# Kernel optimization log

Hardware: AMD Instinct MI355X
Metric: run time of the kernel (lower is better)

The kernel has to match this reference:

```python
import jax, jax.numpy as jnp
import numpy as np

START_TAG = 7
STOP_TAG = 8
NEG = -10000.0  # matches torch.full((1,K), -10000.) in the original


def setup_inputs() -> dict:
    key = jax.random.key(0)
    k1, k2, k3, k4 = jax.random.split(key, 4)
    B, T, K = 1024, 2048, 9  # K = output_dim + 2 (START/STOP hardcoded as 7/8)
    feats = jax.random.normal(k1, (B, T, K), dtype=jnp.float32)
    tags = jax.random.randint(k2, (B, T), 0, 7)            # valid labels 0..6
    lengths = jax.random.randint(k3, (B,), 1, T + 1)        # per-sentence lengths >= 1
    transitions = jax.random.normal(k4, (K, K), dtype=jnp.float32)
    transitions = transitions.at[START_TAG, :].set(NEG)     # never transition into START
    transitions = transitions.at[:, STOP_TAG].set(NEG)      # never transition out of STOP
    return {"feats": feats, "transitions": transitions, "tags": tags, "lengths": lengths}


def _crf_nll(feats, transitions, tags, lengths):
    # feats: [B,T,K] emissions, transitions[j,i] = score of i -> j
    B, T, K = feats.shape

    def fwd_one(feat, length):
        # CRF forward algorithm (log partition), vectorized over tags,
        # lax.scan over time; masked past `length` to emulate feats[:x_len].
        alpha0 = jnp.full((K,), NEG, feat.dtype).at[START_TAG].set(0.0)

        def step(alpha, inp):
            t, f = inp
            # alpha_new[j] = logsumexp_i(alpha[i] + transitions[j,i]) + feat[t,j]
            new = jax.nn.logsumexp(alpha[None, :] + transitions, axis=1) + f
            return jnp.where(t < length, new, alpha), None

        alpha, _ = jax.lax.scan(step, alpha0, (jnp.arange(T), feat))
        return jax.nn.logsumexp(alpha + transitions[STOP_TAG])

    fwd_scores = jax.vmap(fwd_one)(feats, lengths)  # [B]

    def gold_one(feat, tg, length):
        # _score_sentence: sum_t trans[tags[t], tags[t-1]] + feat[t, tags[t]]
        prev = jnp.concatenate([jnp.array([START_TAG], tg.dtype), tg[:-1]])
        step_scores = transitions[tg, prev] + jnp.take_along_axis(feat, tg[:, None], axis=1)[:, 0]
        mask = jnp.arange(tg.shape[0]) < length
        last = tg[length - 1]
        return jnp.sum(jnp.where(mask, step_scores, 0.0)) + transitions[STOP_TAG, last]

    gold_scores = jax.vmap(gold_one)(feats, tags, lengths)  # [B]

    # neg_log_likelihood accumulates (forward - gold) per sentence, then / n
    return jnp.mean(fwd_scores - gold_scores)


def reference(feats, transitions, tags, lengths):
    return _crf_nll(feats, transitions, tags, lengths)
```

## Files before the change

kernel.cpp:

```cpp
#include <hip/hip_runtime.h>


#define START_TAG 7
#define STOP_TAG  8
#define KDIM      9
#define NS        7
#define CPS       64
#define SLICES    8
#define NEGINF    (-1e30f)

__device__ __forceinline__ float rfl(float x) {
    return __int_as_float(__builtin_amdgcn_readfirstlane(__float_as_int(x)));
}

__global__ __launch_bounds__(256, 8) void crf_chunk_kernel(
    const float* __restrict__ feats,
    const float* __restrict__ trans,
    const int*   __restrict__ lengths,
    float* __restrict__ g_seg,
    int B, int T)
{
    __shared__ float s_E[49];
    __shared__ float s_M[4 * 512];

    const int tid = threadIdx.x;
    if (tid < 49) s_E[tid] = __expf(trans[(tid / 7) * 9 + (tid % 7)]);
    __syncthreads();

    const int widx = tid >> 6;
    const int W    = blockIdx.x * 4 + widx;
    const int s    = W / B;
    const int b    = W - s * B;

    const int    len   = lengths[b];
    const float* fbase = feats + (size_t)b * T * KDIM;
    const int    Lb    = (len > 1) ? ((len - 1 + CPS - 1) / CPS) : 1;

    {
        const int lane8  = tid & 7;
        const int k      = (tid >> 3) & 7;
        const int c      = s * 8 + k;
        const int tstart = 1 + c * Lb;
        const int tend   = min(tstart + Lb, len);

        if (lane8 < NS) {
            float* Mw = s_M + widx * 512 + k * 64;
            if (tstart < tend) {
                float E[49];
                #pragma unroll
                for (int e = 0; e < 49; ++e) E[e] = rfl(s_E[e]);

                int baddr[NS];
                #pragma unroll
                for (int j = 0; j < NS; ++j) baddr[j] = (((tid & 56) | j) << 2);

                float p[NS];
                #pragma unroll
                for (int j = 0; j < NS; ++j) p[j] = (j == lane8) ? 1.f : 0.f;
                float sc = 0.f;
                int rem = tend - tstart;

                const float* fp = fbase + (size_t)tstart * KDIM + lane8;

                #define CRF_MAT(EF) do {                                        \
                    float q[NS];                                                \
                    _Pragma("unroll")                                           \
                    for (int j = 0; j < NS; ++j) {                              \
                        float acc = E[j * 7] * p[0];                            \
                        _Pragma("unroll")                                       \
                        for (int i = 1; i < NS; ++i)                            \
                            acc = fmaf(E[j * 7 + i], p[i], acc);                \
                        q[j] = acc;                                             \
                    }                                                           \
                    _Pragma("unroll")                                           \
                    for (int j = 0; j < NS; ++j) p[j] = q[j] * EF[j];           \
                } while (0)

                #define CRF_BCAST(DST, XF) do {                                 \
                    float _e = __expf(XF);                                      \
                    _Pragma("unroll")                                           \
                    for (int j = 0; j < NS; ++j)                                \
                        DST[j] = __int_as_float(                                \
                            __builtin_amdgcn_ds_bpermute(                       \
                                baddr[j], __float_as_int(_e)));                 \
                } while (0)

                #define CRF_STEP(XF) do {                                       \
                    float _ef[NS];                                              \
                    CRF_BCAST(_ef, XF);                                         \
                    CRF_MAT(_ef);                                               \
                } while (0)

                #define CRF_RENORM() do {                                       \
                    float m = p[0];                                             \
                    _Pragma("unroll")                                           \
                    for (int j = 1; j < NS; ++j) m = fmaxf(m, p[j]);            \
                    float rm = __builtin_amdgcn_rcpf(m);                        \
                    _Pragma("unroll")                                           \
                    for (int j = 0; j < NS; ++j) p[j] *= rm;                    \
                    sc += __logf(m);                                            \
                } while (0)

                int o1 = KDIM * min(1, rem - 1);
                int o2 = KDIM * min(2, rem - 1);
                int o3 = KDIM * min(3, rem - 1);
                float x0 = fp[0], x1 = fp[o1], x2 = fp[o2], x3 = fp[o3];
                fp += 4 * KDIM;

                while (rem >= 8) {
                    float y0 = fp[0], y1 = fp[KDIM], y2 = fp[2 * KDIM], y3 = fp[3 * KDIM];
                    fp += 4 * KDIM;
                    float efA[NS], efB[NS], efC[NS], efD[NS];
                    CRF_BCAST(efA, x0);
                    CRF_BCAST(efB, x1);
                    CRF_BCAST(efC, x2);
                    CRF_BCAST(efD, x3);
                    CRF_MAT(efA); CRF_MAT(efB); CRF_MAT(efC); CRF_MAT(efD);
                    CRF_RENORM();
                    x0 = y0; x1 = y1; x2 = y2; x3 = y3;
                    rem -= 4;
                }
                if (rem > 4) {
                    int e1 = KDIM * min(1, rem - 5);
                    int e2 = KDIM * min(2, rem - 5);
                    float y0 = fp[0], y1 = fp[e1], y2 = fp[e2];
                    float efA[NS], efB[NS], efC[NS], efD[NS];
                    CRF_BCAST(efA, x0);
                    CRF_BCAST(efB, x1);
                    CRF_BCAST(efC, x2);
                    CRF_BCAST(efD, x3);
                    CRF_MAT(efA); CRF_MAT(efB); CRF_MAT(efC); CRF_MAT(efD);
                    CRF_RENORM();
                    x0 = y0; x1 = y1; x2 = y2;
                    rem -= 4;
                }
                CRF_STEP(x0);
                if (rem > 1) CRF_STEP(x1);
                if (rem > 2) CRF_STEP(x2);
                if (rem > 3) CRF_STEP(x3);

                #pragma unroll
                for (int j = 0; j < NS; ++j)
                    Mw[j * 8 + lane8] = __logf(p[j]) + sc;

                #undef CRF_MAT
                #undef CRF_BCAST
                #undef CRF_STEP
                #undef CRF_RENORM
            } else {
                #pragma unroll
                for (int j = 0; j < NS; ++j)
                    Mw[j * 8 + lane8] = (j == lane8) ? 0.f : NEGINF;
            }
        }
    }

    asm volatile("s_waitcnt lgkmcnt(0)" ::: "memory");

    {
        const int l  = tid & 63;
        const int i  = l & 7;
        float* sg = s_M + widx * 512;

        float A = sg[l];
        int baddr[NS];
        #pragma unroll
        for (int k = 0; k < NS; ++k) baddr[k] = ((k << 3) | i) << 2;

        #pragma unroll
        for (int c = 1; c < 8; ++c) {
            const float* Mr = sg + c * 64 + (l & 56);
            float4 r0 = *(const float4*)(Mr);
            float4 r1 = *(const float4*)(Mr + 4);
            float ac[NS];
            #pragma unroll
            for (int k = 0; k < NS; ++k)
                ac[k] = __int_as_float(__builtin_amdgcn_ds_bpermute(
                            baddr[k], __float_as_int(A)));
            float t0 = r0.x + ac[0], t1 = r0.y + ac[1], t2 = r0.z + ac[2];
            float t3 = r0.w + ac[3], t4 = r1.x + ac[4], t5 = r1.y + ac[5];
            float t6 = r1.z + ac[6];
            float tm = fmaxf(fmaxf(fmaxf(t0, t1), fmaxf(t2, t3)),
                             fmaxf(fmaxf(t4, t5), t6));
            float sum = ((__expf(t0 - tm) + __expf(t1 - tm)) +
                         (__expf(t2 - tm) + __expf(t3 - tm))) +
                        ((__expf(t4 - tm) + __expf(t5 - tm)) + __expf(t6 - tm));
            A = tm + __logf(sum);
        }
        g_seg[((size_t)(b * SLICES + s)) * 64 + l] = A;
    }
}

__global__ __launch_bounds__(256) void crf_fold_kernel(
    const float* __restrict__ feats,
    const float* __restrict__ trans,
    const int*   __restrict__ tags,
    const int*   __restrict__ lengths,
    const float* __restrict__ g_seg,
    float* __restrict__ out,
    int B, int T)
{
    __shared__ float s_trans[81];
    __shared__ float s_S[512];
    __shared__ float s_gold[4];

    const int tid = threadIdx.x;
    const int b   = blockIdx.x;

    if (tid < 81) s_trans[tid] = trans[tid];
    {
        const float* sp = g_seg + (size_t)b * 512;
        s_S[tid]       = sp[tid];
        s_S[tid + 256] = sp[tid + 256];
    }
    __syncthreads();

    const int    len   = lengths[b];
    const int*   tg    = tags  + (size_t)b * T;
    const float* fbase = feats + (size_t)b * T * KDIM;

    {
        int per = (T >> 8) > 0 ? (T >> 8) : 1;
        int t0  = tid * per;
        float g = 0.f;
        if (t0 < len) {
            int te   = min(t0 + per, len);
            int prev = (t0 == 0) ? START_TAG : tg[t0 - 1];
            if (per == 8) {
                #pragma unroll
                for (int k = 0; k < 8; ++k) {
                    int t   = t0 + k;
                    int tc  = min(t, te - 1);
                    int cur = tg[tc];
                    float v = s_trans[cur * 9 + prev] + fbase[(size_t)tc * KDIM + cur];
                    g += (t < te) ? v : 0.f;
                    prev = cur;
                }
            } else {
                for (int k = 0; k < per; ++k) {
                    int t   = t0 + k;
                    int tc  = min(t, te - 1);
                    int cur = tg[tc];
                    float v = s_trans[cur * 9 + prev] + fbase[(size_t)tc * KDIM + cur];
                    g += (t < te) ? v : 0.f;
                    prev = cur;
                }
            }
            if (len - 1 >= t0 && len - 1 < t0 + per)
                g += s_trans[STOP_TAG * 9 + tg[len - 1]];
        }
        #pragma unroll
        for (int off = 32; off > 0; off >>= 1) g += __shfl_xor(g, off, 64);
        if ((tid & 63) == 0) s_gold[tid >> 6] = g;
    }
    __syncthreads();

    if (tid < 8) {
        const int  lane  = tid;
        const bool isrow = (lane < NS);
        const int  row   = isrow ? lane : 0;

        float a[NS];
        #pragma unroll
        for (int i = 0; i < NS; ++i)
            a[i] = s_trans[i * 9 + START_TAG] + fbase[i];
        float S;
        {
            float mm = fmaxf(fmaxf(fmaxf(a[0], a[1]), fmaxf(a[2], a[3])),
                             fmaxf(fmaxf(a[4], a[5]), a[6]));
            S = mm;
            #pragma unroll
            for (int i = 0; i < NS; ++i) a[i] -= mm;
        }

        const float* Mr0 = s_S + row * 8;
        float4 mA = *(const float4*)(Mr0);
        float4 mB = *(const float4*)(Mr0 + 4);
        #pragma unroll
        for (int w = 0; w < 8; ++w) {
            int wn = min(w + 1, 7);
            float4 nA = *(const float4*)(Mr0 + wn * 64);
            float4 nB = *(const float4*)(Mr0 + wn * 64 + 4);
            float t0 = mA.x + a[0], t1 = mA.y + a[1], t2 = mA.z + a[2];
            float t3 = mA.w + a[3], t4 = mB.x + a[4], t5 = mB.y + a[5];
            float t6 = mB.z + a[6];
            float tm = fmaxf(fmaxf(fmaxf(t0, t1), fmaxf(t2, t3)),
                             fmaxf(fmaxf(t4, t5), t6));
            float e0 = __expf(t0 - tm), e1 = __expf(t1 - tm), e2 = __expf(t2 - tm);
            float e3 = __expf(t3 - tm), e4 = __expf(t4 - tm), e5 = __expf(t5 - tm);
            float e6 = __expf(t6 - tm);
            float sum = ((e0 + e1) + (e2 + e3)) + ((e4 + e5) + e6);
            float na = isrow ? (tm + __logf(sum)) : NEGINF;
            float b0 = __shfl(na, 0, 8), b1 = __shfl(na, 1, 8), b2 = __shfl(na, 2, 8);
            float b3 = __shfl(na, 3, 8), b4 = __shfl(na, 4, 8), b5 = __shfl(na, 5, 8);
            float b6 = __shfl(na, 6, 8);
            float mm = fmaxf(fmaxf(fmaxf(b0, b1), fmaxf(b2, b3)),
                             fmaxf(fmaxf(b4, b5), b6));
            a[0] = b0 - mm; a[1] = b1 - mm; a[2] = b2 - mm;
            a[3] = b3 - mm; a[4] = b4 - mm; a[5] = b5 - mm;
            a[6] = b6 - mm;
            S += mm;
            mA = nA; mB = nB;
        }

        if (lane == 0) {
            float t0 = a[0] + s_trans[STOP_TAG * 9 + 0];
            float t1 = a[1] + s_trans[STOP_TAG * 9 + 1];
            float t2 = a[2] + s_trans[STOP_TAG * 9 + 2];
            float t3 = a[3] + s_trans[STOP_TAG * 9 + 3];
            float t4 = a[4] + s_trans[STOP_TAG * 9 + 4];
            float t5 = a[5] + s_trans[STOP_TAG * 9 + 5];
            float t6 = a[6] + s_trans[STOP_TAG * 9 + 6];
            float tm = fmaxf(fmaxf(fmaxf(t0, t1), fmaxf(t2, t3)),
                             fmaxf(fmaxf(t4, t5), t6));
            float sum = ((__expf(t0 - tm) + __expf(t1 - tm)) +
                         (__expf(t2 - tm) + __expf(t3 - tm))) +
                        ((__expf(t4 - tm) + __expf(t5 - tm)) + __expf(t6 - tm));
            float fwd = S + tm + __logf(sum);
            float g = s_gold[0] + s_gold[1] + s_gold[2] + s_gold[3];
            atomicAdd(out, (fwd - g) * (1.0f / (float)B));
        }
    }
}

__global__ void init_out_kernel(float* out) {
    if (threadIdx.x == 0) out[0] = 0.f;
}

extern "C" void kernel_launch(void* const* d_in, const int* in_sizes, int n_in,
                              void* d_out, int out_size, void* d_ws, size_t ws_size,
                              hipStream_t stream) {
    const float* feats   = (const float*)d_in[0];
    const float* trans   = (const float*)d_in[1];
    const int*   tags    = (const int*)d_in[2];
    const int*   lengths = (const int*)d_in[3];

    int B = in_sizes[3];
    int T = in_sizes[2] / B;

    float* seg = (float*)d_ws;

    init_out_kernel<<<1, 64, 0, stream>>>((float*)d_out);
    crf_chunk_kernel<<<B * SLICES / 4, 256, 0, stream>>>(
        feats, trans, lengths, seg, B, T);
    crf_fold_kernel<<<B, 256, 0, stream>>>(
        feats, trans, tags, lengths, seg, (float*)d_out, B, T);
}
```

Before: 164.9 us.

## Move gold-path score computation into chunk kernel and slim fold kernel

The gold sentence score is now computed per (batch, slice) inside the chunk kernel, with one wavefront per slice summing its time range and writing a partial to workspace. The fold kernel shrinks to a 64-thread block that only loads segment matrices, reduces the eight gold partials with shuffles, and runs the serial fold. This takes the gold gather off the fold kernel's critical path and overlaps it with the chunk kernel's work. In exchange, the chunk kernel's occupancy hint drops from 8 to 4 blocks, and it gains extra loads and registers that may slow its main scan.

```diff
diff --git a/kernel.cpp b/kernel.cpp
--- a/kernel.cpp
+++ b/kernel.cpp
@@ -13,18 +13,25 @@
     return __int_as_float(__builtin_amdgcn_readfirstlane(__float_as_int(x)));
 }
 
-__global__ __launch_bounds__(256, 8) void crf_chunk_kernel(
+__global__ __launch_bounds__(256, 4) void crf_chunk_kernel(
     const float* __restrict__ feats,
     const float* __restrict__ trans,
+    const int*   __restrict__ tags,
     const int*   __restrict__ lengths,
     float* __restrict__ g_seg,
+    float* __restrict__ g_gold,
     int B, int T)
 {
+    __shared__ float s_trans[81];
     __shared__ float s_E[49];
     __shared__ float s_M[4 * 512];
 
     const int tid = threadIdx.x;
-    if (tid < 49) s_E[tid] = __expf(trans[(tid / 7) * 9 + (tid % 7)]);
+    if (tid < 81) s_trans[tid] = trans[tid];
+    if (tid >= 128 && tid < 177) {
+        int k = tid - 128;
+        s_E[k] = __expf(trans[(k / 7) * 9 + (k % 7)]);
+    }
     __syncthreads();
 
     const int widx = tid >> 6;
@@ -33,8 +40,37 @@
     const int b    = W - s * B;
 
     const int    len   = lengths[b];
+    const int*   tg    = tags  + (size_t)b * T;
     const float* fbase = feats + (size_t)b * T * KDIM;
     const int    Lb    = (len > 1) ? ((len - 1 + CPS - 1) / CPS) : 1;
+
+    {
+        const int gs = (s == 0) ? 0 : 1 + s * 8 * Lb;
+        const int ge = (s == SLICES - 1) ? len : min(1 + (s + 1) * 8 * Lb, len);
+        float g = 0.f;
+        if (gs < ge) {
+            int span = ge - gs;
+            int per  = (span + 63) >> 6;
+            int t0   = gs + (tid & 63) * per;
+            if (t0 < ge) {
+                int te   = min(t0 + per, ge);
+                int prev = (t0 == 0) ? START_TAG : tg[t0 - 1];
+                for (int k = 0; k < per; ++k) {
+                    int t   = t0 + k;
+                    int tc  = min(t, te - 1);
+                    int cur = tg[tc];
+                    float v = s_trans[cur * 9 + prev] + fbase[(size_t)tc * KDIM + cur];
+                    g += (t < te) ? v : 0.f;
+                    prev = cur;
+                }
+                if (len - 1 >= t0 && len - 1 < t0 + per && len - 1 < ge)
+                    g += s_trans[STOP_TAG * 9 + tg[len - 1]];
+            }
+        }
+        #pragma unroll
+        for (int off = 32; off > 0; off >>= 1) g += __shfl_xor(g, off, 64);
+        if ((tid & 63) == 0) g_gold[b * SLICES + s] = g;
+    }
 
     {
         const int lane8  = tid & 7;
@@ -191,79 +227,40 @@
     }
 }
 
-__global__ __launch_bounds__(256) void crf_fold_kernel(
+__global__ __launch_bounds__(64) void crf_fold_kernel(
     const float* __restrict__ feats,
     const float* __restrict__ trans,
-    const int*   __restrict__ tags,
-    const int*   __restrict__ lengths,
     const float* __restrict__ g_seg,
+    const float* __restrict__ g_gold,
     float* __restrict__ out,
     int B, int T)
 {
-    __shared__ float s_trans[81];
     __shared__ float s_S[512];
-    __shared__ float s_gold[4];
 
     const int tid = threadIdx.x;
     const int b   = blockIdx.x;
 
-    if (tid < 81) s_trans[tid] = trans[tid];
     {
         const float* sp = g_seg + (size_t)b * 512;
-        s_S[tid]       = sp[tid];
-        s_S[tid + 256] = sp[tid + 256];
-    }
-    __syncthreads();
-
-    const int    len   = lengths[b];
-    const int*   tg    = tags  + (size_t)b * T;
-    const float* fbase = feats + (size_t)b * T * KDIM;
-
-    {
-        int per = (T >> 8) > 0 ? (T >> 8) : 1;
-        int t0  = tid * per;
-        float g = 0.f;
-        if (t0 < len) {
-            int te   = min(t0 + per, len);
-            int prev = (t0 == 0) ? START_TAG : tg[t0 - 1];
-            if (per == 8) {
-                #pragma unroll
-                for (int k = 0; k < 8; ++k) {
-                    int t   = t0 + k;
-                    int tc  = min(t, te - 1);
-                    int cur = tg[tc];
-                    float v = s_trans[cur * 9 + prev] + fbase[(size_t)tc * KDIM + cur];
-                    g += (t < te) ? v : 0.f;
-                    prev = cur;
-                }
-            } else {
-                for (int k = 0; k < per; ++k) {
-                    int t   = t0 + k;
-                    int tc  = min(t, te - 1);
-                    int cur = tg[tc];
-                    float v = s_trans[cur * 9 + prev] + fbase[(size_t)tc * KDIM + cur];
-                    g += (t < te) ? v : 0.f;
-                    prev = cur;
-                }
-            }
-            if (len - 1 >= t0 && len - 1 < t0 + per)
-                g += s_trans[STOP_TAG * 9 + tg[len - 1]];
-        }
-        #pragma unroll
-        for (int off = 32; off > 0; off >>= 1) g += __shfl_xor(g, off, 64);
-        if ((tid & 63) == 0) s_gold[tid >> 6] = g;
-    }
+        #pragma unroll
+        for (int k = 0; k < 8; ++k) s_S[tid + 64 * k] = sp[tid + 64 * k];
+    }
+    float gg = (tid < 8) ? g_gold[b * SLICES + tid] : 0.f;
+    gg += __shfl_xor(gg, 1, 8);
+    gg += __shfl_xor(gg, 2, 8);
+    gg += __shfl_xor(gg, 4, 8);
     __syncthreads();
 
     if (tid < 8) {
         const int  lane  = tid;
         const bool isrow = (lane < NS);
         const int  row   = isrow ? lane : 0;
+        const float* fbase = feats + (size_t)b * T * KDIM;
 
         float a[NS];
         #pragma unroll
         for (int i = 0; i < NS; ++i)
-            a[i] = s_trans[i * 9 + START_TAG] + fbase[i];
+            a[i] = trans[i * 9 + START_TAG] + fbase[i];
         float S;
         {
             float mm = fmaxf(fmaxf(fmaxf(a[0], a[1]), fmaxf(a[2], a[3])),
@@ -304,21 +301,20 @@
         }
 
         if (lane == 0) {
-            float t0 = a[0] + s_trans[STOP_TAG * 9 + 0];
-            float t1 = a[1] + s_trans[STOP_TAG * 9 + 1];
-            float t2 = a[2] + s_trans[STOP_TAG * 9 + 2];
-            float t3 = a[3] + s_trans[STOP_TAG * 9 + 3];
-            float t4 = a[4] + s_trans[STOP_TAG * 9 + 4];
-            float t5 = a[5] + s_trans[STOP_TAG * 9 + 5];
-            float t6 = a[6] + s_trans[STOP_TAG * 9 + 6];
+            float t0 = a[0] + trans[STOP_TAG * 9 + 0];
+            float t1 = a[1] + trans[STOP_TAG * 9 + 1];
+            float t2 = a[2] + trans[STOP_TAG * 9 + 2];
+            float t3 = a[3] + trans[STOP_TAG * 9 + 3];
+            float t4 = a[4] + trans[STOP_TAG * 9 + 4];
+            float t5 = a[5] + trans[STOP_TAG * 9 + 5];
+            float t6 = a[6] + trans[STOP_TAG * 9 + 6];
             float tm = fmaxf(fmaxf(fmaxf(t0, t1), fmaxf(t2, t3)),
                              fmaxf(fmaxf(t4, t5), t6));
             float sum = ((__expf(t0 - tm) + __expf(t1 - tm)) +
                          (__expf(t2 - tm) + __expf(t3 - tm))) +
                         ((__expf(t4 - tm) + __expf(t5 - tm)) + __expf(t6 - tm));
             float fwd = S + tm + __logf(sum);
-            float g = s_gold[0] + s_gold[1] + s_gold[2] + s_gold[3];
-            atomicAdd(out, (fwd - g) * (1.0f / (float)B));
+            atomicAdd(out, (fwd - gg) * (1.0f / (float)B));
         }
     }
 }
@@ -338,11 +334,12 @@
     int B = in_sizes[3];
     int T = in_sizes[2] / B;
 
-    float* seg = (float*)d_ws;
+    float* seg  = (float*)d_ws;
+    float* gold = seg + (size_t)B * SLICES * 64;
 
     init_out_kernel<<<1, 64, 0, stream>>>((float*)d_out);
     crf_chunk_kernel<<<B * SLICES / 4, 256, 0, stream>>>(
-        feats, trans, lengths, seg, B, T);
-    crf_fold_kernel<<<B, 256, 0, stream>>>(
-        feats, trans, tags, lengths, seg, (float*)d_out, B, T);
-}
+        feats, trans, tags, lengths, seg, gold, B, T);
+    crf_fold_kernel<<<B, 64, 0, stream>>>(
+        feats, trans, seg, gold, (float*)d_out, B, T);
+}
```

After: 154.1 us. -6.6%, faster.
